# Kernel tuning notes

Hardware: AMD Instinct MI355X
Metric: run time of the kernel (lower is better)

## Reference

```python
import jax, jax.numpy as jnp
import numpy as np

EMBED = 1024
HEADS = 16
HEAD_DIM = EMBED // HEADS
N, L, S = 16, 256, 2


def setup_inputs() -> dict:
    key = jax.random.key(0)
    ks = jax.random.split(key, 9)
    values = jax.random.normal(ks[0], (N, L, EMBED, S), dtype=jnp.float32)
    keys_ = jax.random.normal(ks[1], (N, L, EMBED, S), dtype=jnp.float32)
    query = jax.random.normal(ks[2], (N, L, EMBED, S), dtype=jnp.float32)
    mask = jax.random.randint(ks[3], (N, S, EMBED, L), 0, 2, dtype=jnp.int32)
    # nn.Linear weights: y = x @ W.T (+ b)
    sc = 1.0 / np.sqrt(HEAD_DIM)
    Wv = jax.random.uniform(ks[4], (HEAD_DIM, HEAD_DIM), jnp.float32, -sc, sc)
    Wk = jax.random.uniform(ks[5], (HEAD_DIM, HEAD_DIM), jnp.float32, -sc, sc)
    Wq = jax.random.uniform(ks[6], (HEAD_DIM, HEAD_DIM), jnp.float32, -sc, sc)
    so = 1.0 / np.sqrt(EMBED)
    Wo = jax.random.uniform(ks[7], (EMBED, EMBED), jnp.float32, -so, so)
    bo = jax.random.uniform(ks[8], (EMBED,), jnp.float32, -so, so)
    return {"values": values, "keys": keys_, "query": query, "mask": mask,
            "Wv": Wv, "Wk": Wk, "Wq": Wq, "Wo": Wo, "bo": bo}


def reference(values, keys, query, mask, Wv, Wk, Wq, Wo, bo):
    n, L, E, S = values.shape
    H, D = HEADS, HEAD_DIM
    # reshape exactly as torch (memory reinterpretation): (n, len, S, H, D)
    v = values.reshape(n, L, S, H, D)
    k = keys.reshape(n, L, S, H, D)
    q = query.reshape(n, L, S, H, D)
    # per-head linear projections (no bias): x @ W.T
    v = jnp.einsum('nlshd,ed->nlshe', v, Wv)
    k = jnp.einsum('nlshd,ed->nlshe', k, Wk)
    q = jnp.einsum('nlshd,ed->nlshe', q, Wq)
    energy = jnp.einsum('nqshd,nkshd->nhsqk', q, k)
    # mask: (n, S, E, L) -> take feature 0 -> (n, S, L) -> repeat heads -> (n, H, S, L)
    m = mask.reshape(n, S, E, L)[:, :, 0, :]              # (n, S, L)
    m = jnp.tile(m[..., None], (1, 1, 1, H))               # (n, S, L, H)
    m = m.reshape(n, H, S, L)                              # as torch reshape
    energy = jnp.where(m[..., None] == 0, jnp.float32(-1e20), energy)
    # NOTE: original softmaxes over dim=3 (query axis) — replicate faithfully
    att = jax.nn.softmax(energy / jnp.sqrt(jnp.float32(E)), axis=3)
    out = jnp.einsum('nhsql,nlshd->nqhds', att, v)         # (n, q, H, D, S)
    out = out.reshape(n, L, S, H * D)                      # torch-style reshape
    return jnp.einsum('nqse,fe->nqsf', out, Wo) + bo
```

## Files before the change

### kernel.cpp

```cpp
#include <hip/hip_runtime.h>


typedef __attribute__((ext_vector_type(8))) short bf16x8;
typedef __attribute__((ext_vector_type(4))) float f32x4;

__device__ inline ushort f2bf(float x) {
    uint u = __float_as_uint(x);
    u += 0x7FFFu + ((u >> 16) & 1u);
    return (ushort)(u >> 16);
}

__global__ __launch_bounds__(256) void k_wot(
    const float* __restrict__ Wo, ushort* __restrict__ Wb)
{
    const int f = blockIdx.x;
    const int e4 = threadIdx.x * 4;
    const int hr = e4 >> 7, sp = (e4 >> 6) & 1, d = e4 & 63;
    const float* wrow = Wo + (long)f * 1024 + hr * 128 + 2 * d + sp;
    ushort o[4] = {f2bf(wrow[0]), f2bf(wrow[2]), f2bf(wrow[4]), f2bf(wrow[6])};
    *(uint2*)(Wb + (long)f * 1024 + e4) = *(uint2*)o;
}

__global__ __launch_bounds__(256) void k_proj(
    const float* __restrict__ Av, const float* __restrict__ Ak,
    const float* __restrict__ Aq, const float* __restrict__ Wv,
    const float* __restrict__ Wk, const float* __restrict__ Wq,
    ushort* __restrict__ kB, ushort* __restrict__ qB,
    ushort* __restrict__ vB)
{
    __shared__ ushort As[256][72];
    __shared__ ushort Ws[64][72];
    const int b = blockIdx.x;
    const int n = b >> 5, h = (b >> 1) & 15, s = b & 1;
    const float* Asrc[3] = {Av, Ak, Aq};
    const float* Wsrc[3] = {Wv, Wk, Wq};
    const int tid = threadIdx.x;
    const int wid = tid >> 6, lane = tid & 63;
    const int lr = lane & 15, lk = lane >> 4;

    const long abase = (long)n * 524288 + s * 1024 + h * 64;
    const long slice = ((long)((n * 16 + h) * 2 + s)) * 16384;
    ushort* Bdst[3] = {vB, kB, qB};

#pragma unroll 1
    for (int m = 0; m < 3; ++m) {
        __syncthreads();
#pragma unroll
        for (int w = 0; w < 16; ++w) {
            int idx = w * 256 + tid;
            int r = idx >> 4, c4 = (idx & 15) * 4;
            float4 v = *(const float4*)(Asrc[m] + abase + (long)r * 2048 + c4);
            ushort t4[4] = {f2bf(v.x), f2bf(v.y), f2bf(v.z), f2bf(v.w)};
            *(uint2*)&As[r][c4] = *(uint2*)t4;
        }
#pragma unroll
        for (int w = 0; w < 4; ++w) {
            int idx = w * 256 + tid;
            int r = idx >> 4, c4 = (idx & 15) * 4;
            float4 v = *(const float4*)(Wsrc[m] + r * 64 + c4);
            ushort t4[4] = {f2bf(v.x), f2bf(v.y), f2bf(v.z), f2bf(v.w)};
            *(uint2*)&Ws[r][c4] = *(uint2*)t4;
        }
        __syncthreads();

        f32x4 acc[4][4];
#pragma unroll
        for (int lt = 0; lt < 4; ++lt)
#pragma unroll
            for (int et = 0; et < 4; ++et)
#pragma unroll
                for (int rg = 0; rg < 4; ++rg) acc[lt][et][rg] = 0.f;

#pragma unroll
        for (int ks = 0; ks < 2; ++ks) {
            bf16x8 a[4], bb[4];
#pragma unroll
            for (int lt = 0; lt < 4; ++lt)
                a[lt] = *(const bf16x8*)
                    &As[wid * 64 + lt * 16 + lr][ks * 32 + lk * 8];
#pragma unroll
            for (int et = 0; et < 4; ++et)
                bb[et] = *(const bf16x8*)
                    &Ws[et * 16 + lr][ks * 32 + lk * 8];
#pragma unroll
            for (int lt = 0; lt < 4; ++lt)
#pragma unroll
                for (int et = 0; et < 4; ++et)
                    acc[lt][et] = __builtin_amdgcn_mfma_f32_16x16x32_bf16(
                        a[lt], bb[et], acc[lt][et], 0, 0, 0);
        }

#pragma unroll
        for (int lt = 0; lt < 4; ++lt)
#pragma unroll
            for (int et = 0; et < 4; ++et)
#pragma unroll
                for (int rg = 0; rg < 4; ++rg) {
                    const int l = wid * 64 + lt * 16 + lk * 4 + rg;
                    const int e = et * 16 + lr;
                    Bdst[m][slice + (long)l * 64 + e] = f2bf(acc[lt][et][rg]);
                }
    }
}

__global__ __launch_bounds__(512) void k_attn(
    const ushort* __restrict__ kB, const ushort* __restrict__ qB,
    const ushort* __restrict__ vB, const int* __restrict__ mask,
    ushort* __restrict__ Xb)
{
    __shared__ ushort Ks[32][72];
    __shared__ ushort vsT[64][44];
    __shared__ ushort Es[128][44];
    __shared__ float Zl[256];
    __shared__ int mb16[16];
    const int nhs = blockIdx.x;
    const int n = nhs >> 5, h = (nhs >> 1) & 15, s = nhs & 1;
    const long slice = (long)nhs * 16384;
    const int tid = threadIdx.x;
    const int wid = tid >> 6, lane = tid & 63;
    const int lr = lane & 15, lk = lane >> 4;

    bf16x8 aq[2][2];
#pragma unroll
    for (int qt = 0; qt < 2; ++qt) {
        const int qb = wid * 32 + qt * 16;
        aq[qt][0] = *(const bf16x8*)(qB + slice + (qb + lr) * 64 + lk * 8);
        aq[qt][1] = *(const bf16x8*)(qB + slice + (qb + lr) * 64 + 32 + lk * 8);
    }
    const int mrow = n * 524288 + (h >> 3) * 262144 + (h & 7) * 32 + s * 16;
    if (tid < 16) mb16[tid] = mask[mrow + tid];
    if (tid < 256) Zl[tid] = 0.f;

    const float scale = 0.03125f;

#pragma unroll 1
    for (int sl = 0; sl < 8; ++sl) {
        __syncthreads();
        if (tid < 256) {
            int r = tid >> 3, c8 = (tid & 7) * 8;
            *(uint4*)&Ks[r][c8] =
                *(const uint4*)(kB + slice + (sl * 32 + r) * 64 + c8);
        }
        __syncthreads();

        float zlt[2] = {0.f, 0.f};
#pragma unroll
        for (int qt = 0; qt < 2; ++qt) {
            const int qb = wid * 32 + qt * 16;
            if (mb16[qb >> 4] == 0) continue;
#pragma unroll
            for (int lt = 0; lt < 2; ++lt) {
                f32x4 sacc;
#pragma unroll
                for (int rg = 0; rg < 4; ++rg) sacc[rg] = 0.f;
                bf16x8 b0 = *(const bf16x8*)&Ks[lt * 16 + lr][lk * 8];
                bf16x8 b1 = *(const bf16x8*)&Ks[lt * 16 + lr][32 + lk * 8];
                sacc = __builtin_amdgcn_mfma_f32_16x16x32_bf16(
                    aq[qt][0], b0, sacc, 0, 0, 0);
                sacc = __builtin_amdgcn_mfma_f32_16x16x32_bf16(
                    aq[qt][1], b1, sacc, 0, 0, 0);
#pragma unroll
                for (int rg = 0; rg < 4; ++rg)
                    zlt[lt] += __expf(sacc[rg] * scale);
            }
        }
#pragma unroll
        for (int lt = 0; lt < 2; ++lt) {
            float v = zlt[lt];
            v += __shfl_xor(v, 16);
            v += __shfl_xor(v, 32);
            if (lk == 0)
                atomicAdd(&Zl[sl * 32 + lt * 16 + lr], v);
        }
    }

    __syncthreads();
    if (tid < 256) {
        float z = Zl[tid];
        Zl[tid] = (z > 0.f) ? 1.0f / z : 1.0f / 256.0f;
    }

    f32x4 acc0[4], acc1[4];
#pragma unroll
    for (int dt = 0; dt < 4; ++dt)
#pragma unroll
        for (int rg = 0; rg < 4; ++rg) { acc0[dt][rg] = 0.f; acc1[dt][rg] = 0.f; }

#pragma unroll 1
    for (int sl = 0; sl < 8; ++sl) {
        __syncthreads();
        if (tid < 256) {
            int r = tid >> 3, c8 = (tid & 7) * 8;
            *(uint4*)&Ks[r][c8] =
                *(const uint4*)(kB + slice + (sl * 32 + r) * 64 + c8);
        } else {
            int t = tid - 256;
            int l = t >> 3, d8 = (t & 7) * 8;
            uint4 vv = *(const uint4*)(vB + slice + (sl * 32 + l) * 64 + d8);
            ushort t8[8];
            *(uint4*)t8 = vv;
#pragma unroll
            for (int u = 0; u < 8; ++u) vsT[d8 + u][l] = t8[u];
        }
        __syncthreads();

#pragma unroll
        for (int qt = 0; qt < 2; ++qt) {
            const int qb = wid * 32 + qt * 16;
            const bool live = (mb16[qb >> 4] != 0);
#pragma unroll
            for (int lt = 0; lt < 2; ++lt) {
                f32x4 sacc;
#pragma unroll
                for (int rg = 0; rg < 4; ++rg) sacc[rg] = 0.f;
                bf16x8 b0 = *(const bf16x8*)&Ks[lt * 16 + lr][lk * 8];
                bf16x8 b1 = *(const bf16x8*)&Ks[lt * 16 + lr][32 + lk * 8];
                sacc = __builtin_amdgcn_mfma_f32_16x16x32_bf16(
                    aq[qt][0], b0, sacc, 0, 0, 0);
                sacc = __builtin_amdgcn_mfma_f32_16x16x32_bf16(
                    aq[qt][1], b1, sacc, 0, 0, 0);
                const int l = lt * 16 + lr;
                const float iz = Zl[sl * 32 + l];
#pragma unroll
                for (int rg = 0; rg < 4; ++rg) {
                    float ev = live ? __expf(sacc[rg] * scale) * iz : 0.f;
                    Es[wid * 16 + lk * 4 + rg][l] = f2bf(ev);
                }
            }
            __builtin_amdgcn_s_waitcnt(0);
            bf16x8 aP = *(const bf16x8*)&Es[wid * 16 + lr][lk * 8];
            f32x4* accp = (qt == 0) ? acc0 : acc1;
#pragma unroll
            for (int dt = 0; dt < 4; ++dt) {
                bf16x8 bV = *(const bf16x8*)&vsT[dt * 16 + lr][lk * 8];
                accp[dt] = __builtin_amdgcn_mfma_f32_16x16x32_bf16(
                    aP, bV, accp[dt], 0, 0, 0);
            }
        }
    }

#pragma unroll
    for (int qt = 0; qt < 2; ++qt) {
        const f32x4* accp = (qt == 0) ? acc0 : acc1;
        const int qb = wid * 32 + qt * 16;
#pragma unroll
        for (int dt = 0; dt < 4; ++dt) {
#pragma unroll
            for (int rg = 0; rg < 4; ++rg) {
                const int q = qb + lk * 4 + rg;
                const int d = dt * 16 + lr;
                Xb[slice + (long)q * 64 + d] = f2bf(accp[dt][rg]);
            }
        }
    }
}

__global__ __launch_bounds__(512) void k_wo(
    const ushort* __restrict__ Xb, const ushort* __restrict__ Wb,
    const float* __restrict__ bo, float* __restrict__ out)
{
    __shared__ ushort Xs[128][72];
    __shared__ ushort Ws[128][72];
    const int b = blockIdx.x;
    const int by = b >> 3, bx = b & 7;
    const int r0 = by * 128, f0 = bx * 128;
    const int tid = threadIdx.x;
    const int wid = tid >> 6, lane = tid & 63;
    const int wr = wid >> 2, wc = wid & 3;
    const int lr = lane & 15, lk = lane >> 4;

    f32x4 acc[4][2];
#pragma unroll
    for (int rt = 0; rt < 4; ++rt)
#pragma unroll
        for (int ft = 0; ft < 2; ++ft)
#pragma unroll
            for (int rg = 0; rg < 4; ++rg) acc[rt][ft][rg] = 0.f;

    const int sr = tid >> 2, sc = (tid & 3) * 16;
    const int sR = r0 + sr;
    const int sn = sR >> 9, sq = (sR >> 1) & 255, ss2 = sR & 1;

#pragma unroll 1
    for (int eo = 0; eo < 1024; eo += 64) {
        const int hr = eo >> 7, sp = (eo >> 6) & 1;
        __syncthreads();
        {
            long xo = ((long)((sn * 16 + (ss2 * 8 + hr)) * 2 + sp)) * 16384 +
                      sq * 64 + sc;
            *(uint4*)&Xs[sr][sc] = *(const uint4*)(Xb + xo);
            *(uint4*)&Xs[sr][sc + 8] = *(const uint4*)(Xb + xo + 8);
            long wo = (long)(f0 + sr) * 1024 + eo + sc;
            *(uint4*)&Ws[sr][sc] = *(const uint4*)(Wb + wo);
            *(uint4*)&Ws[sr][sc + 8] = *(const uint4*)(Wb + wo + 8);
        }
        __syncthreads();

#pragma unroll
        for (int ks = 0; ks < 2; ++ks) {
            bf16x8 a[4], bb[2];
#pragma unroll
            for (int rt = 0; rt < 4; ++rt)
                a[rt] = *(const bf16x8*)
                    &Xs[wr * 64 + rt * 16 + lr][ks * 32 + lk * 8];
#pragma unroll
            for (int ft = 0; ft < 2; ++ft)
                bb[ft] = *(const bf16x8*)
                    &Ws[wc * 32 + ft * 16 + lr][ks * 32 + lk * 8];
#pragma unroll
            for (int rt = 0; rt < 4; ++rt)
#pragma unroll
                for (int ft = 0; ft < 2; ++ft)
                    acc[rt][ft] = __builtin_amdgcn_mfma_f32_16x16x32_bf16(
                        a[rt], bb[ft], acc[rt][ft], 0, 0, 0);
        }
    }

#pragma unroll
    for (int ft = 0; ft < 2; ++ft) {
        const int f = f0 + wc * 32 + ft * 16 + lr;
        const float bias = bo[f];
#pragma unroll
        for (int rt = 0; rt < 4; ++rt) {
#pragma unroll
            for (int rg = 0; rg < 4; ++rg) {
                const int r = r0 + wr * 64 + rt * 16 + lk * 4 + rg;
                out[(long)r * 1024 + f] = acc[rt][ft][rg] + bias;
            }
        }
    }
}

extern "C" void kernel_launch(void* const* d_in, const int* in_sizes, int n_in,
                              void* d_out, int out_size, void* d_ws,
                              size_t ws_size, hipStream_t stream)
{
    const float* vals = (const float*)d_in[0];
    const float* keys = (const float*)d_in[1];
    const float* qrys = (const float*)d_in[2];
    const int*   mask = (const int*)d_in[3];
    const float* Wv   = (const float*)d_in[4];
    const float* Wk   = (const float*)d_in[5];
    const float* Wq   = (const float*)d_in[6];
    const float* Wo   = (const float*)d_in[7];
    const float* bo   = (const float*)d_in[8];
    float* ws  = (float*)d_ws;
    ushort* kB = (ushort*)(ws);
    ushort* qB = (ushort*)(ws + 4194304);
    ushort* vB = (ushort*)(ws + 8388608);
    ushort* Xb = (ushort*)(ws + 12582912);
    ushort* Wb = (ushort*)(ws + 16777216);
    float* out = (float*)d_out;

    k_wot <<<1024, 256, 0, stream>>>(Wo, Wb);
    k_proj<<< 512, 256, 0, stream>>>(vals, keys, qrys, Wv, Wk, Wq, kB, qB, vB);
    k_attn<<< 512, 512, 0, stream>>>(kB, qB, vB, mask, Xb);
    k_wo  <<< 512, 512, 0, stream>>>(Xb, Wb, bo, out);
}
```

Before: 104.3 us.

## Load projection activations directly into MFMA fragments and stage all weights once

The projection kernel no longer stages each 256x64 activation tile through shared memory. Each lane now loads its fp32 activation row segment straight from global memory into a bf16 MFMA operand, and all three weight matrices are staged in shared memory once under a single barrier. The MFMA operands are swapped so the output comes out transposed, letting each lane write four contiguous bf16 values as a single 8-byte store instead of scattered 2-byte stores. This removes per-matrix barriers and LDS traffic, at the cost of less coalesced global loads, since each lane reads 32 bytes from a different row.

```diff
diff --git a/kernel.cpp b/kernel.cpp
--- a/kernel.cpp
+++ b/kernel.cpp
@@ -28,8 +28,7 @@
     ushort* __restrict__ kB, ushort* __restrict__ qB,
     ushort* __restrict__ vB)
 {
-    __shared__ ushort As[256][72];
-    __shared__ ushort Ws[64][72];
+    __shared__ ushort Wsb[3][64][72];
     const int b = blockIdx.x;
     const int n = b >> 5, h = (b >> 1) & 15, s = b & 1;
     const float* Asrc[3] = {Av, Ak, Aq};
@@ -42,64 +41,54 @@
     const long slice = ((long)((n * 16 + h) * 2 + s)) * 16384;
     ushort* Bdst[3] = {vB, kB, qB};
 
-#pragma unroll 1
-    for (int m = 0; m < 3; ++m) {
-        __syncthreads();
-#pragma unroll
-        for (int w = 0; w < 16; ++w) {
-            int idx = w * 256 + tid;
-            int r = idx >> 4, c4 = (idx & 15) * 4;
-            float4 v = *(const float4*)(Asrc[m] + abase + (long)r * 2048 + c4);
-            ushort t4[4] = {f2bf(v.x), f2bf(v.y), f2bf(v.z), f2bf(v.w)};
-            *(uint2*)&As[r][c4] = *(uint2*)t4;
-        }
+#pragma unroll
+    for (int m = 0; m < 3; ++m)
 #pragma unroll
         for (int w = 0; w < 4; ++w) {
             int idx = w * 256 + tid;
             int r = idx >> 4, c4 = (idx & 15) * 4;
             float4 v = *(const float4*)(Wsrc[m] + r * 64 + c4);
             ushort t4[4] = {f2bf(v.x), f2bf(v.y), f2bf(v.z), f2bf(v.w)};
-            *(uint2*)&Ws[r][c4] = *(uint2*)t4;
-        }
-        __syncthreads();
-
-        f32x4 acc[4][4];
-#pragma unroll
-        for (int lt = 0; lt < 4; ++lt)
-#pragma unroll
-            for (int et = 0; et < 4; ++et)
-#pragma unroll
-                for (int rg = 0; rg < 4; ++rg) acc[lt][et][rg] = 0.f;
-
-#pragma unroll
-        for (int ks = 0; ks < 2; ++ks) {
-            bf16x8 a[4], bb[4];
-#pragma unroll
-            for (int lt = 0; lt < 4; ++lt)
-                a[lt] = *(const bf16x8*)
-                    &As[wid * 64 + lt * 16 + lr][ks * 32 + lk * 8];
-#pragma unroll
-            for (int et = 0; et < 4; ++et)
-                bb[et] = *(const bf16x8*)
-                    &Ws[et * 16 + lr][ks * 32 + lk * 8];
-#pragma unroll
-            for (int lt = 0; lt < 4; ++lt)
-#pragma unroll
-                for (int et = 0; et < 4; ++et)
-                    acc[lt][et] = __builtin_amdgcn_mfma_f32_16x16x32_bf16(
-                        a[lt], bb[et], acc[lt][et], 0, 0, 0);
-        }
-
-#pragma unroll
-        for (int lt = 0; lt < 4; ++lt)
-#pragma unroll
-            for (int et = 0; et < 4; ++et)
-#pragma unroll
-                for (int rg = 0; rg < 4; ++rg) {
-                    const int l = wid * 64 + lt * 16 + lk * 4 + rg;
-                    const int e = et * 16 + lr;
-                    Bdst[m][slice + (long)l * 64 + e] = f2bf(acc[lt][et][rg]);
+            *(uint2*)&Wsb[m][r][c4] = *(uint2*)t4;
+        }
+    __syncthreads();
+
+    const int l0 = wid * 64;
+#pragma unroll 1
+    for (int m = 0; m < 3; ++m) {
+        const float* A = Asrc[m];
+        ushort* B = Bdst[m];
+#pragma unroll
+        for (int lt = 0; lt < 4; ++lt) {
+            const int lrow = l0 + lt * 16 + lr;
+            const float* arow = A + abase + (long)lrow * 2048;
+            bf16x8 bfrag[2];
+#pragma unroll
+            for (int ks = 0; ks < 2; ++ks) {
+                float4 v0 = *(const float4*)(arow + ks * 32 + lk * 8);
+                float4 v1 = *(const float4*)(arow + ks * 32 + lk * 8 + 4);
+                ushort t8[8] = {f2bf(v0.x), f2bf(v0.y), f2bf(v0.z), f2bf(v0.w),
+                                f2bf(v1.x), f2bf(v1.y), f2bf(v1.z), f2bf(v1.w)};
+                bfrag[ks] = *(bf16x8*)t8;
+            }
+#pragma unroll
+            for (int et = 0; et < 4; ++et) {
+                f32x4 acc;
+#pragma unroll
+                for (int rg = 0; rg < 4; ++rg) acc[rg] = 0.f;
+#pragma unroll
+                for (int ks = 0; ks < 2; ++ks) {
+                    bf16x8 wfrag = *(const bf16x8*)
+                        &Wsb[m][et * 16 + lr][ks * 32 + lk * 8];
+                    acc = __builtin_amdgcn_mfma_f32_16x16x32_bf16(
+                        wfrag, bfrag[ks], acc, 0, 0, 0);
                 }
+                ushort t4[4] = {f2bf(acc[0]), f2bf(acc[1]),
+                                f2bf(acc[2]), f2bf(acc[3])};
+                *(uint2*)(B + slice + (long)lrow * 64 + et * 16 + lk * 4) =
+                    *(uint2*)t4;
+            }
+        }
     }
 }
 
```

New measurement: 97.62 us. 1.07x faster.
